# Kernel tuning notes

Hardware: AMD Instinct MI355X
Metric: run time of the kernel (lower is better)

The kernel has to match this reference:

```python
import jax, jax.numpy as jnp
import numpy as np

B, T, C, H = 4, 2048, 1024, 16

def setup_inputs() -> dict:
    key = jax.random.key(0)
    k1, k2, k3, k4, k5 = jax.random.split(key, 5)
    s = 1.0 / np.sqrt(C)
    return {
        "x": jax.random.normal(k1, (B, T, C), dtype=jnp.float32),
        "w_attn": jax.random.normal(k2, (C, 3 * C), dtype=jnp.float32) * s,
        "b_attn": jax.random.normal(k3, (3 * C,), dtype=jnp.float32) * 0.02,
        "w_proj": jax.random.normal(k4, (C, C), dtype=jnp.float32) * s,
        "b_proj": jax.random.normal(k5, (C,), dtype=jnp.float32) * 0.02,
    }

def reference(x, w_attn, b_attn, w_proj, b_proj):
    Bx, Tx, Cx = x.shape
    hd = Cx // H  # head_size
    qkv = x @ w_attn + b_attn                      # [B,T,3C]
    q, k, v = jnp.split(qkv, 3, axis=2)
    # [B,T,C] -> [B,H,T,hd]
    def heads(t):
        return t.reshape(Bx, Tx, H, hd).transpose(0, 2, 1, 3)
    q, k, v = heads(q), heads(k), heads(v)
    scale = hd ** -0.5
    scores = jnp.einsum("bhqd,bhkd->bhqk", q, k) * scale  # [B,H,T,T]
    causal = jnp.tril(jnp.ones((Tx, Tx), dtype=bool))
    scores = jnp.where(causal[None, None], scores, -jnp.inf)
    probs = jax.nn.softmax(scores, axis=-1)
    attn = jnp.einsum("bhqk,bhkd->bhqd", probs, v)  # [B,H,T,hd]
    attn = attn.transpose(0, 2, 1, 3).reshape(Bx, Tx, Cx)
    return attn @ w_proj + b_proj
```

## Files before the change

### kernel.cpp

```cpp
#include <hip/hip_runtime.h>
#include <hip/hip_bf16.h>

#define BATCH 4
#define TSEQ  2048
#define CDIM  1024
#define NHEAD 16
#define HDIM  64
#define C3    3072
#define MROWS (BATCH * TSEQ)

#define QSCALE 0.18033688011112f

typedef short bf16x8 __attribute__((ext_vector_type(8)));
typedef short short8 __attribute__((ext_vector_type(8)));
typedef __bf16 bf16v8 __attribute__((ext_vector_type(8)));
typedef float f32x4 __attribute__((ext_vector_type(4)));

#define AS1 __attribute__((address_space(1)))
#define AS3 __attribute__((address_space(3)))

#if __has_builtin(__builtin_amdgcn_exp2f)
#define EXP2F(x) __builtin_amdgcn_exp2f(x)
#else
#define EXP2F(x) exp2f(x)
#endif

__device__ __forceinline__ short f2bf(float x) {
    unsigned int u = __builtin_bit_cast(unsigned int, x);
    u += 0x7fffu + ((u >> 16) & 1u);
    return (short)(u >> 16);
}

__device__ __forceinline__ unsigned int cvtpk(float lo, float hi) {
    unsigned int r;
    asm("v_cvt_pk_bf16_f32 %0, %1, %2" : "=v"(r) : "v"(lo), "v"(hi));
    return r;
}

__device__ __forceinline__ f32x4 mfma16(bf16x8 a, bf16x8 b, f32x4 c) {
    return __builtin_amdgcn_mfma_f32_16x16x32_bf16(
        __builtin_bit_cast(bf16v8, a), __builtin_bit_cast(bf16v8, b), c, 0, 0, 0);
}

__global__ void f32_to_bf16_kernel(const float* __restrict__ in,
                                   short* __restrict__ out, int n8) {
    int i = blockIdx.x * blockDim.x + threadIdx.x;
    if (i >= n8) return;
    float4 a = ((const float4*)in)[2 * i];
    float4 b = ((const float4*)in)[2 * i + 1];
    short8 o;
    o[0] = f2bf(a.x); o[1] = f2bf(a.y); o[2] = f2bf(a.z); o[3] = f2bf(a.w);
    o[4] = f2bf(b.x); o[5] = f2bf(b.y); o[6] = f2bf(b.z); o[7] = f2bf(b.w);
    ((short8*)out)[i] = o;
}

__global__ void transpose2_kernel(const float* __restrict__ wA,
                                  short* __restrict__ wAT,
                                  const float* __restrict__ wP,
                                  short* __restrict__ wPT, float qs) {
    const float* in;
    short* out;
    int N, qcols;
    float sc;
    if (blockIdx.z == 0) { in = wA; out = wAT; N = C3; qcols = CDIM; sc = qs; }
    else {
        if (blockIdx.x >= CDIM / 32) return;
        in = wP; out = wPT; N = CDIM; qcols = 0; sc = 1.0f;
    }
    __shared__ float tile[32][33];
    const int n0 = blockIdx.x * 32, k0 = blockIdx.y * 32;
    const int tx = threadIdx.x, ty = threadIdx.y;
#pragma unroll
    for (int j = 0; j < 4; ++j)
        tile[ty + j * 8][tx] = in[(size_t)(k0 + ty + j * 8) * N + n0 + tx];
    __syncthreads();
#pragma unroll
    for (int j = 0; j < 4; ++j) {
        const int n = n0 + ty + j * 8;
        const float s = (n < qcols) ? sc : 1.0f;
        out[(size_t)n * CDIM + k0 + tx] = f2bf(tile[tx][ty + j * 8] * s);
    }
}

template <typename OutT, int WAVES_M, int WAVES_N, int BN>
__global__ __launch_bounds__(512, 4) void gemm3_kernel(
    const short* __restrict__ A, const short* __restrict__ Bt,
    const float* __restrict__ bias, OutT* __restrict__ out,
    int M, int N, int K, int qcols, float qs) {
    constexpr int BM = 128;
    constexpr int MF = BM / (WAVES_M * 16);
    constexpr int NF = BN / (WAVES_N * 16);
    constexpr int BLOADS = BN / 128;
    __shared__ alignas(16) short Ab[3][BM * 32];
    __shared__ alignas(16) short Bb[3][BN * 32];

    const int tid = threadIdx.x;
    const int lane = tid & 63;
    const int w = tid >> 6;
    const int wm = w / WAVES_N;
    const int wn = w % WAVES_N;

    const int nwg = gridDim.x * gridDim.y;
    const int lid = blockIdx.y * gridDim.x + blockIdx.x;
    const int swz = (lid & 7) * (nwg >> 3) + (lid >> 3);
    const int m0 = (swz / gridDim.x) * BM;
    const int n0 = (swz % gridDim.x) * BN;

    const int NT = K >> 5;

    const int fr = lane & 15;
    const int ch = lane >> 4;

    f32x4 acc[MF][NF] = {};

    const int rA  = tid >> 2;
    const int lcA = (tid & 3) ^ ((rA >> 1) & 3);
    const short* gA = A + (size_t)(m0 + rA) * K + lcA * 8;
    const short* gB[BLOADS];
#pragma unroll
    for (int i = 0; i < BLOADS; ++i) {
        const int s = tid + i * 512;
        const int r = s >> 2;
        const int lc = (s & 3) ^ ((r >> 1) & 3);
        gB[i] = Bt + (size_t)(n0 + r) * K + lc * 8;
    }

    int aoff[MF], boff[NF];
#pragma unroll
    for (int f = 0; f < MF; ++f) {
        const int r = wm * (BM / WAVES_M) + f * 16 + fr;
        aoff[f] = r * 32 + (ch ^ ((r >> 1) & 3)) * 8;
    }
#pragma unroll
    for (int f = 0; f < NF; ++f) {
        const int r = wn * (BN / WAVES_N) + f * 16 + fr;
        boff[f] = r * 32 + (ch ^ ((r >> 1) & 3)) * 8;
    }

#define GSTAGE(buf, kt)                                                          \
    do {                                                                         \
        __builtin_amdgcn_global_load_lds((const AS1 void*)(gA + (kt)),           \
            (AS3 void*)&Ab[buf][w * 512], 16, 0, 0);                             \
        _Pragma("unroll")                                                        \
        for (int i = 0; i < BLOADS; ++i)                                         \
            __builtin_amdgcn_global_load_lds((const AS1 void*)(gB[i] + (kt)),    \
                (AS3 void*)&Bb[buf][i * 4096 + w * 512], 16, 0, 0);              \
    } while (0)

#define GITER(BUF, T)                                                            \
    do {                                                                         \
        if constexpr (BLOADS == 2) {                                             \
            asm volatile("s_waitcnt vmcnt(3)" ::: "memory");                     \
        } else {                                                                 \
            asm volatile("s_waitcnt vmcnt(2)" ::: "memory");                     \
        }                                                                        \
        __builtin_amdgcn_s_barrier();                                            \
        const int ktn = (((T) + 2 < NT) ? ((T) + 2) : 0) * 32;                   \
        GSTAGE((BUF + 2) % 3, ktn);                                              \
        __builtin_amdgcn_sched_barrier(0);                                       \
        bf16x8 af[MF], bfv[NF];                                                  \
        _Pragma("unroll")                                                        \
        for (int f = 0; f < MF; ++f)                                             \
            af[f] = *(const bf16x8*)&Ab[BUF][aoff[f]];                           \
        _Pragma("unroll")                                                        \
        for (int f = 0; f < NF; ++f)                                             \
            bfv[f] = *(const bf16x8*)&Bb[BUF][boff[f]];                          \
        _Pragma("unroll")                                                        \
        for (int mf = 0; mf < MF; ++mf)                                          \
            _Pragma("unroll")                                                    \
            for (int nf = 0; nf < NF; ++nf)                                      \
                acc[mf][nf] = mfma16(af[mf], bfv[nf], acc[mf][nf]);              \
    } while (0)

    GSTAGE(0, 0);
    GSTAGE(1, 32);

    int t = 0;
    for (; t + 3 <= NT; t += 3) {
        GITER(0, t);
        GITER(1, t + 1);
        GITER(2, t + 2);
    }
    if (t < NT) { GITER(0, t); ++t; }
    if (t < NT) { GITER(1, t); }
#undef GITER
#undef GSTAGE

    const int r0 = (lane >> 4) * 4;
    const int cn = lane & 15;
#pragma unroll
    for (int mf = 0; mf < MF; ++mf) {
#pragma unroll
        for (int nf = 0; nf < NF; ++nf) {
            const int col = n0 + wn * (BN / WAVES_N) + nf * 16 + cn;
            const float bv = bias[col] * ((col < qcols) ? qs : 1.0f);
#pragma unroll
            for (int r = 0; r < 4; ++r) {
                const int row = m0 + wm * (BM / WAVES_M) + mf * 16 + r0 + r;
                const float v = acc[mf][nf][r] + bv;
                if constexpr (sizeof(OutT) == 2)
                    out[(size_t)row * N + col] = (OutT)f2bf(v);
                else
                    out[(size_t)row * N + col] = (OutT)v;
            }
        }
    }
}

template <int BUF>
__device__ __forceinline__ void attn_iter(
    int KB, int niter, int qrow, int w, int cn, int g, int kg8,
    int krow, int kx0, int kx1, int skv, int sd0,
    const short* kgl, size_t ksrc, const short* vbase,
    short (*klds)[64 * 64], short (*vt)[64 * 72],
    const bf16x8 (&qf)[2][2], f32x4 (&ao)[2][4], f32x4 (&ao4)[2],
    const bf16x8& vones) {

    const int kvb = KB * 64;
    const bool pf = (KB + 1 < niter);

    bf16x8 r0, r1;
    if (pf) {
        r0 = *(const bf16x8*)(vbase + (size_t)(kvb + 64 + skv) * C3 + sd0);
        r1 = *(const bf16x8*)(vbase + (size_t)(kvb + 64 + skv + 1) * C3 + sd0);
        const short* kn = kgl + ksrc + (size_t)(kvb + 64) * C3;
        __builtin_amdgcn_global_load_lds((const AS1 void*)kn,
            (AS3 void*)&klds[BUF ^ 1][w * 512], 16, 0, 0);
        __builtin_amdgcn_global_load_lds((const AS1 void*)(kn + (size_t)32 * C3),
            (AS3 void*)&klds[BUF ^ 1][2048 + w * 512], 16, 0, 0);
    }

    if (kvb <= qrow + 31) {
        bf16x8 kf[4][2];
#pragma unroll
        for (int t = 0; t < 4; ++t) {
            const int rb = t * 1024 + krow;
            kf[t][0] = *(const bf16x8*)&klds[BUF][rb + kx0];
            kf[t][1] = *(const bf16x8*)&klds[BUF][rb + kx1];
        }

        bf16x8 vf[2][4];
#pragma unroll
        for (int c = 0; c < 2; ++c)
#pragma unroll
            for (int dt = 0; dt < 4; ++dt)
                vf[c][dt] = *(const bf16x8*)&vt[BUF][(dt * 16 + cn) * 72 + c * 32 + kg8];

#pragma unroll
        for (int qt = 0; qt < 2; ++qt) {
            const int qrow16 = qrow + qt * 16;

            f32x4 s[4] = {};
#pragma unroll
            for (int t = 0; t < 4; ++t) {
                s[t] = mfma16(kf[t][0], qf[qt][0], s[t]);
                s[t] = mfma16(kf[t][1], qf[qt][1], s[t]);
            }

            const bool maskIter = (kvb + 63 > qrow16);
            float p[4][4];
            if (maskIter) {
#pragma unroll
                for (int t = 0; t < 4; ++t)
#pragma unroll
                    for (int r = 0; r < 4; ++r) {
                        const int kv = kvb + t * 16 + 4 * g + r;
                        const int q  = qrow16 + cn;
                        float e = EXP2F(s[t][r]);
                        p[t][r] = (kv > q) ? 0.f : e;
                    }
            } else {
#pragma unroll
                for (int t = 0; t < 4; ++t)
#pragma unroll
                    for (int r = 0; r < 4; ++r)
                        p[t][r] = EXP2F(s[t][r]);
            }

            unsigned int wq[8];
#pragma unroll
            for (int t = 0; t < 4; ++t) {
                wq[t * 2 + 0] = cvtpk(p[t][0], p[t][1]);
                wq[t * 2 + 1] = cvtpk(p[t][2], p[t][3]);
            }

#pragma unroll
            for (int c = 0; c < 2; ++c) {
                union { unsigned int u[4]; bf16x8 v; } pu;
                unsigned int p0 = wq[4 * c + 0], p2 = wq[4 * c + 2];
                asm("v_permlane32_swap_b32 %0, %1" : "+v"(p0), "+v"(p2));
                asm("v_permlane16_swap_b32 %0, %1" : "+v"(p0), "+v"(p2));
                pu.u[0] = p0; pu.u[2] = p2;
                unsigned int p1 = wq[4 * c + 1], p3 = wq[4 * c + 3];
                asm("v_permlane32_swap_b32 %0, %1" : "+v"(p1), "+v"(p3));
                asm("v_permlane16_swap_b32 %0, %1" : "+v"(p1), "+v"(p3));
                pu.u[1] = p1; pu.u[3] = p3;
#pragma unroll
                for (int dt = 0; dt < 4; ++dt)
                    ao[qt][dt] = mfma16(pu.v, vf[c][dt], ao[qt][dt]);
                ao4[qt] = mfma16(pu.v, vones, ao4[qt]);
            }
        }
    }

    if (pf) {
#pragma unroll
        for (int i = 0; i < 8; ++i) {
            unsigned int pk = (unsigned short)r0[i] | ((unsigned int)(unsigned short)r1[i] << 16);
            *(unsigned int*)&vt[BUF ^ 1][(sd0 + i) * 72 + skv] = pk;
        }
    }
    __syncthreads();
}

__global__ __launch_bounds__(256) void attn_kernel(const short* __restrict__ qkv,
                                                   short* __restrict__ attn_out) {
    __shared__ short vt[2][64 * 72];
    __shared__ short klds[2][64 * 64];

    const int tid = threadIdx.x;
    const int lane = tid & 63;
    const int w = tid >> 6;

    const int bid = blockIdx.x;
    const int swz = (bid & 7) * 64 + (bid >> 3);
    const int bh = swz >> 3;
    const int pairp = swz & 7;
    const int b = bh >> 4;
    const int h = bh & 15;

    const size_t base = (size_t)b * TSEQ * C3 + (size_t)h * HDIM;
    const int cn = lane & 15;
    const int g = lane >> 4;
    const int kg8 = g * 8;

    const bf16x8 vones = {0x3F80, 0x3F80, 0x3F80, 0x3F80,
                          0x3F80, 0x3F80, 0x3F80, 0x3F80};

    const short* kgl = qkv + base + 1024;
    const size_t ksrc = (size_t)(w * 8 + (lane >> 3)) * C3 + ((lane & 7) ^ (lane >> 3)) * 8;
    const int cnl = cn & 7;
    const int krow = cn * 64;
    const int kx0 = ((g ^ cnl) * 8);
    const int kx1 = (((g ^ 4) ^ cnl) * 8);

    const int skv = (tid & 31) * 2;
    const int sd0 = (tid >> 5) * 8;
    const short* vbase = qkv + base + 2048;

    for (int pass = 0; pass < 2; ++pass) {
        const int qi = pass ? pairp : (15 - pairp);
        const int q0 = qi * 128;
        const int qrow = q0 + w * 32;
        const int niter = 2 * qi + 2;

        bf16x8 qf[2][2];
#pragma unroll
        for (int qt = 0; qt < 2; ++qt)
#pragma unroll
            for (int ks = 0; ks < 2; ++ks)
                qf[qt][ks] = *(const bf16x8*)(qkv + base +
                    (size_t)(qrow + qt * 16 + cn) * C3 + ks * 32 + kg8);

        f32x4 ao[2][4] = {};
        f32x4 ao4[2] = {};

        {
            __builtin_amdgcn_global_load_lds((const AS1 void*)(kgl + ksrc),
                                             (AS3 void*)&klds[0][w * 512], 16, 0, 0);
            __builtin_amdgcn_global_load_lds((const AS1 void*)(kgl + ksrc + (size_t)32 * C3),
                                             (AS3 void*)&klds[0][2048 + w * 512], 16, 0, 0);
            bf16x8 r0 = *(const bf16x8*)(vbase + (size_t)skv * C3 + sd0);
            bf16x8 r1 = *(const bf16x8*)(vbase + (size_t)(skv + 1) * C3 + sd0);
#pragma unroll
            for (int i = 0; i < 8; ++i) {
                unsigned int pk = (unsigned short)r0[i] | ((unsigned int)(unsigned short)r1[i] << 16);
                *(unsigned int*)&vt[0][(sd0 + i) * 72 + skv] = pk;
            }
        }
        __syncthreads();

        int kb = 0;
        for (; kb + 2 <= niter; kb += 2) {
            attn_iter<0>(kb,     niter, qrow, w, cn, g, kg8, krow, kx0, kx1,
                         skv, sd0, kgl, ksrc, vbase, klds, vt, qf, ao, ao4, vones);
            attn_iter<1>(kb + 1, niter, qrow, w, cn, g, kg8, krow, kx0, kx1,
                         skv, sd0, kgl, ksrc, vbase, klds, vt, qf, ao, ao4, vones);
        }

#pragma unroll
        for (int qt = 0; qt < 2; ++qt) {
#pragma unroll
            for (int r = 0; r < 4; ++r) {
                const float lr = 1.0f / ao4[qt][r];
                const int q = qrow + qt * 16 + 4 * g + r;
#pragma unroll
                for (int dt = 0; dt < 4; ++dt)
                    attn_out[(size_t)(b * TSEQ + q) * CDIM + h * HDIM + dt * 16 + cn] =
                        f2bf(ao[qt][dt][r] * lr);
            }
        }
        __syncthreads();
    }
}

extern "C" void kernel_launch(void* const* d_in, const int* in_sizes, int n_in,
                              void* d_out, int out_size, void* d_ws, size_t ws_size,
                              hipStream_t stream) {
    const float* x      = (const float*)d_in[0];
    const float* w_attn = (const float*)d_in[1];
    const float* b_attn = (const float*)d_in[2];
    const float* w_proj = (const float*)d_in[3];
    const float* b_proj = (const float*)d_in[4];
    float* out = (float*)d_out;

    char* ws = (char*)d_ws;
    short* x_bf   = (short*)ws;
    short* wqkvT  = (short*)(ws + (16u << 20));
    short* wprojT = (short*)(ws + (22u << 20));
    short* qkv    = (short*)(ws + (24u << 20));

    f32_to_bf16_kernel<<<(MROWS * CDIM / 8 + 255) / 256, 256, 0, stream>>>(x, x_bf, MROWS * CDIM / 8);
    transpose2_kernel<<<dim3(C3 / 32, CDIM / 32, 2), dim3(32, 8), 0, stream>>>(
        w_attn, wqkvT, w_proj, wprojT, QSCALE);

    gemm3_kernel<short, 2, 4, 256><<<dim3(C3 / 256, MROWS / 128), 512, 0, stream>>>(
        x_bf, wqkvT, b_attn, qkv, MROWS, C3, CDIM, CDIM, QSCALE);

    attn_kernel<<<dim3(512), 256, 0, stream>>>(qkv, x_bf);

    gemm3_kernel<float, 4, 2, 128><<<dim3(CDIM / 128, MROWS / 128), 512, 0, stream>>>(
        x_bf, wprojT, b_proj, out, MROWS, CDIM, CDIM, 0, 1.0f);
}
```

Measured before the change: 160.0 us.

## Add 256x128-tile GEMM kernel with workgroup swizzle for QKV projection

Adds a new GEMM kernel with 4 waves per 256-thread block, each computing a 128x64 sub-tile (8x4 MFMA fragments) of a 256x128 block tile. Loading uses triple-buffered direct global-to-LDS copies with XOR swizzling. Block indices are remapped with a modulo-8 swizzle for cache locality. The QKV projection now uses it in place of the 512-thread 128x256 kernel, aiming for more register-level reuse per wave. The cost is much higher register pressure and fewer waves per CU.

```diff
diff --git a/kernel.cpp b/kernel.cpp
--- a/kernel.cpp
+++ b/kernel.cpp
@@ -82,6 +82,130 @@
     }
 }
 
+template <typename OutT>
+__global__ __launch_bounds__(256, 2) void gemm4_kernel(
+    const short* __restrict__ A, const short* __restrict__ Bt,
+    const float* __restrict__ bias, OutT* __restrict__ out,
+    int M, int N, int K, int qcols, float qs) {
+    constexpr int MF = 8, NF = 4;
+    __shared__ alignas(16) short Ab[3][256 * 32];
+    __shared__ alignas(16) short Bb[3][128 * 32];
+
+    const int tid = threadIdx.x;
+    const int lane = tid & 63;
+    const int w = tid >> 6;
+    const int wm = w >> 1, wn = w & 1;
+
+    const int nwg = gridDim.x * gridDim.y;
+    const int lid = blockIdx.y * gridDim.x + blockIdx.x;
+    const int swz = (lid & 7) * (nwg >> 3) + (lid >> 3);
+    const int m0 = (swz / gridDim.x) * 256;
+    const int n0 = (swz % gridDim.x) * 128;
+
+    const int NT = K >> 5;
+
+    const int fr = lane & 15;
+    const int ch = lane >> 4;
+
+    f32x4 acc[MF][NF] = {};
+
+    const short* gA[4];
+#pragma unroll
+    for (int i = 0; i < 4; ++i) {
+        const int s = tid + i * 256;
+        const int r = s >> 2;
+        const int lc = (s & 3) ^ ((r >> 1) & 3);
+        gA[i] = A + (size_t)(m0 + r) * K + lc * 8;
+    }
+    const short* gB[2];
+#pragma unroll
+    for (int i = 0; i < 2; ++i) {
+        const int s = tid + i * 256;
+        const int r = s >> 2;
+        const int lc = (s & 3) ^ ((r >> 1) & 3);
+        gB[i] = Bt + (size_t)(n0 + r) * K + lc * 8;
+    }
+
+    int aoff[MF], boff[NF];
+#pragma unroll
+    for (int f = 0; f < MF; ++f) {
+        const int r = wm * 128 + f * 16 + fr;
+        aoff[f] = r * 32 + (ch ^ ((r >> 1) & 3)) * 8;
+    }
+#pragma unroll
+    for (int f = 0; f < NF; ++f) {
+        const int r = wn * 64 + f * 16 + fr;
+        boff[f] = r * 32 + (ch ^ ((r >> 1) & 3)) * 8;
+    }
+
+#define G4STAGE(buf, kt)                                                         \
+    do {                                                                         \
+        _Pragma("unroll")                                                        \
+        for (int i = 0; i < 4; ++i)                                              \
+            __builtin_amdgcn_global_load_lds((const AS1 void*)(gA[i] + (kt)),    \
+                (AS3 void*)&Ab[buf][i * 2048 + w * 512], 16, 0, 0);              \
+        _Pragma("unroll")                                                        \
+        for (int i = 0; i < 2; ++i)                                              \
+            __builtin_amdgcn_global_load_lds((const AS1 void*)(gB[i] + (kt)),    \
+                (AS3 void*)&Bb[buf][i * 2048 + w * 512], 16, 0, 0);              \
+    } while (0)
+
+#define G4ITER(BUF, T)                                                           \
+    do {                                                                         \
+        asm volatile("s_waitcnt vmcnt(6)" ::: "memory");                         \
+        __builtin_amdgcn_s_barrier();                                            \
+        const int ktn = (((T) + 2 < NT) ? ((T) + 2) : 0) * 32;                   \
+        G4STAGE((BUF + 2) % 3, ktn);                                             \
+        __builtin_amdgcn_sched_barrier(0);                                       \
+        bf16x8 af[MF], bfv[NF];                                                  \
+        _Pragma("unroll")                                                        \
+        for (int f = 0; f < MF; ++f)                                             \
+            af[f] = *(const bf16x8*)&Ab[BUF][aoff[f]];                           \
+        _Pragma("unroll")                                                        \
+        for (int f = 0; f < NF; ++f)                                             \
+            bfv[f] = *(const bf16x8*)&Bb[BUF][boff[f]];                          \
+        _Pragma("unroll")                                                        \
+        for (int mf = 0; mf < MF; ++mf)                                          \
+            _Pragma("unroll")                                                    \
+            for (int nf = 0; nf < NF; ++nf)                                      \
+                acc[mf][nf] = mfma16(af[mf], bfv[nf], acc[mf][nf]);              \
+    } while (0)
+
+    G4STAGE(0, 0);
+    G4STAGE(1, 32);
+
+    int t = 0;
+    for (; t + 3 <= NT; t += 3) {
+        G4ITER(0, t);
+        G4ITER(1, t + 1);
+        G4ITER(2, t + 2);
+    }
+    if (t < NT) { G4ITER(0, t); ++t; }
+    if (t < NT) { G4ITER(1, t); }
+#undef G4ITER
+#undef G4STAGE
+
+    const int r0 = (lane >> 4) * 4;
+    const int cn = lane & 15;
+#pragma unroll
+    for (int mf = 0; mf < MF; ++mf) {
+#pragma unroll
+        for (int nf = 0; nf < NF; ++nf) {
+            const int col = n0 + wn * 64 + nf * 16 + cn;
+            const float bv = bias[col] * ((col < qcols) ? qs : 1.0f);
+#pragma unroll
+            for (int r = 0; r < 4; ++r) {
+                const int row = m0 + wm * 128 + mf * 16 + r0 + r;
+                const float v = acc[mf][nf][r] + bv;
+                if constexpr (sizeof(OutT) == 2)
+                    out[(size_t)row * N + col] = (OutT)f2bf(v);
+                else
+                    out[(size_t)row * N + col] = (OutT)v;
+            }
+        }
+    }
+}
+
 template <typename OutT, int WAVES_M, int WAVES_N, int BN>
 __global__ __launch_bounds__(512, 4) void gemm3_kernel(
     const short* __restrict__ A, const short* __restrict__ Bt,
@@ -424,7 +548,7 @@
     transpose2_kernel<<<dim3(C3 / 32, CDIM / 32, 2), dim3(32, 8), 0, stream>>>(
         w_attn, wqkvT, w_proj, wprojT, QSCALE);
 
-    gemm3_kernel<short, 2, 4, 256><<<dim3(C3 / 256, MROWS / 128), 512, 0, stream>>>(
+    gemm4_kernel<short><<<dim3(C3 / 128, MROWS / 256), 256, 0, stream>>>(
         x_bf, wqkvT, b_attn, qkv, MROWS, C3, CDIM, CDIM, QSCALE);
 
     attn_kernel<<<dim3(512), 256, 0, stream>>>(qkv, x_bf);
```

Result: slower. 163.9 us (+2.5%).

## Restructure attention to 2-wave blocks with 64 query rows per wave; merge prep kernels

Applied to the files above, without the earlier changes.

The attention kernel now launches 1024 blocks of 128 threads, each handling one 128-row query tile with two waves covering 64 rows each, instead of 512 blocks of 4 waves that each processed a paired heavy and light tile in two passes. Each wave now keeps four 16-row query fragments and accumulators, which doubles K/V reuse per LDS load but raises register pressure, and each thread loads twice as much K/V per stage. Blocks are ordered with the heaviest causal tiles first so the scheduler can balance the load. The x-to-bf16 conversion and the weight transposes are merged into one prep launch to save a kernel launch.

```diff
diff --git a/kernel.cpp b/kernel.cpp
--- a/kernel.cpp
+++ b/kernel.cpp
@@ -42,34 +42,34 @@
         __builtin_bit_cast(bf16v8, a), __builtin_bit_cast(bf16v8, b), c, 0, 0, 0);
 }
 
-__global__ void f32_to_bf16_kernel(const float* __restrict__ in,
-                                   short* __restrict__ out, int n8) {
-    int i = blockIdx.x * blockDim.x + threadIdx.x;
-    if (i >= n8) return;
-    float4 a = ((const float4*)in)[2 * i];
-    float4 b = ((const float4*)in)[2 * i + 1];
-    short8 o;
-    o[0] = f2bf(a.x); o[1] = f2bf(a.y); o[2] = f2bf(a.z); o[3] = f2bf(a.w);
-    o[4] = f2bf(b.x); o[5] = f2bf(b.y); o[6] = f2bf(b.z); o[7] = f2bf(b.w);
-    ((short8*)out)[i] = o;
-}
-
-__global__ void transpose2_kernel(const float* __restrict__ wA,
-                                  short* __restrict__ wAT,
-                                  const float* __restrict__ wP,
-                                  short* __restrict__ wPT, float qs) {
+__global__ void prep_kernel(const float* __restrict__ x, short* __restrict__ x_bf,
+                            const float* __restrict__ wA, short* __restrict__ wAT,
+                            const float* __restrict__ wP, short* __restrict__ wPT,
+                            float qs) {
+    const int tx = threadIdx.x, ty = threadIdx.y;
+    if (blockIdx.z == 0) {
+        const int i = (blockIdx.y * 128 + blockIdx.x) * 256 + ty * 32 + tx;
+        float4 a = ((const float4*)x)[2 * i];
+        float4 b = ((const float4*)x)[2 * i + 1];
+        short8 o;
+        o[0] = f2bf(a.x); o[1] = f2bf(a.y); o[2] = f2bf(a.z); o[3] = f2bf(a.w);
+        o[4] = f2bf(b.x); o[5] = f2bf(b.y); o[6] = f2bf(b.z); o[7] = f2bf(b.w);
+        ((short8*)x_bf)[i] = o;
+        return;
+    }
     const float* in;
     short* out;
     int N, qcols;
     float sc;
-    if (blockIdx.z == 0) { in = wA; out = wAT; N = C3; qcols = CDIM; sc = qs; }
-    else {
+    if (blockIdx.z == 1) {
+        if (blockIdx.x >= C3 / 32) return;
+        in = wA; out = wAT; N = C3; qcols = CDIM; sc = qs;
+    } else {
         if (blockIdx.x >= CDIM / 32) return;
         in = wP; out = wPT; N = CDIM; qcols = 0; sc = 1.0f;
     }
     __shared__ float tile[32][33];
     const int n0 = blockIdx.x * 32, k0 = blockIdx.y * 32;
-    const int tx = threadIdx.x, ty = threadIdx.y;
 #pragma unroll
     for (int j = 0; j < 4; ++j)
         tile[ty + j * 8][tx] = in[(size_t)(k0 + ty + j * 8) * N + n0 + tx];
@@ -213,24 +213,28 @@
     int krow, int kx0, int kx1, int skv, int sd0,
     const short* kgl, size_t ksrc, const short* vbase,
     short (*klds)[64 * 64], short (*vt)[64 * 72],
-    const bf16x8 (&qf)[2][2], f32x4 (&ao)[2][4], f32x4 (&ao4)[2],
+    const bf16x8 (&qf)[4][2], f32x4 (&ao)[4][4], f32x4 (&ao4)[4],
     const bf16x8& vones) {
 
     const int kvb = KB * 64;
     const bool pf = (KB + 1 < niter);
 
-    bf16x8 r0, r1;
+    bf16x8 r0, r1, r2, r3;
     if (pf) {
-        r0 = *(const bf16x8*)(vbase + (size_t)(kvb + 64 + skv) * C3 + sd0);
-        r1 = *(const bf16x8*)(vbase + (size_t)(kvb + 64 + skv + 1) * C3 + sd0);
+        const short* vn = vbase + (size_t)(kvb + 64) * C3;
+        r0 = *(const bf16x8*)(vn + (size_t)skv * C3 + sd0);
+        r1 = *(const bf16x8*)(vn + (size_t)(skv + 1) * C3 + sd0);
+        r2 = *(const bf16x8*)(vn + (size_t)skv * C3 + sd0 + 32);
+        r3 = *(const bf16x8*)(vn + (size_t)(skv + 1) * C3 + sd0 + 32);
         const short* kn = kgl + ksrc + (size_t)(kvb + 64) * C3;
-        __builtin_amdgcn_global_load_lds((const AS1 void*)kn,
-            (AS3 void*)&klds[BUF ^ 1][w * 512], 16, 0, 0);
-        __builtin_amdgcn_global_load_lds((const AS1 void*)(kn + (size_t)32 * C3),
-            (AS3 void*)&klds[BUF ^ 1][2048 + w * 512], 16, 0, 0);
-    }
-
-    if (kvb <= qrow + 31) {
+#pragma unroll
+        for (int c = 0; c < 4; ++c)
+            __builtin_amdgcn_global_load_lds(
+                (const AS1 void*)(kn + (size_t)(c * 16) * C3),
+                (AS3 void*)&klds[BUF ^ 1][c * 1024 + w * 512], 16, 0, 0);
+    }
+
+    if (kvb <= qrow + 63) {
         bf16x8 kf[4][2];
 #pragma unroll
         for (int t = 0; t < 4; ++t) {
@@ -247,7 +251,7 @@
                 vf[c][dt] = *(const bf16x8*)&vt[BUF][(dt * 16 + cn) * 72 + c * 32 + kg8];
 
 #pragma unroll
-        for (int qt = 0; qt < 2; ++qt) {
+        for (int qt = 0; qt < 4; ++qt) {
             const int qrow16 = qrow + qt * 16;
 
             f32x4 s[4] = {};
@@ -306,14 +310,16 @@
     if (pf) {
 #pragma unroll
         for (int i = 0; i < 8; ++i) {
-            unsigned int pk = (unsigned short)r0[i] | ((unsigned int)(unsigned short)r1[i] << 16);
-            *(unsigned int*)&vt[BUF ^ 1][(sd0 + i) * 72 + skv] = pk;
+            unsigned int pkA = (unsigned short)r0[i] | ((unsigned int)(unsigned short)r1[i] << 16);
+            unsigned int pkB = (unsigned short)r2[i] | ((unsigned int)(unsigned short)r3[i] << 16);
+            *(unsigned int*)&vt[BUF ^ 1][(sd0 + i) * 72 + skv] = pkA;
+            *(unsigned int*)&vt[BUF ^ 1][(sd0 + 32 + i) * 72 + skv] = pkB;
         }
     }
     __syncthreads();
 }
 
-__global__ __launch_bounds__(256) void attn_kernel(const short* __restrict__ qkv,
+__global__ __launch_bounds__(128) void attn_kernel(const short* __restrict__ qkv,
                                                    short* __restrict__ attn_out) {
     __shared__ short vt[2][64 * 72];
     __shared__ short klds[2][64 * 64];
@@ -323,9 +329,8 @@
     const int w = tid >> 6;
 
     const int bid = blockIdx.x;
-    const int swz = (bid & 7) * 64 + (bid >> 3);
-    const int bh = swz >> 3;
-    const int pairp = swz & 7;
+    const int qi = 15 - (bid >> 6);
+    const int bh = (bid & 7) * 8 + ((bid >> 3) & 7);
     const int b = bh >> 4;
     const int h = bh & 15;
 
@@ -348,59 +353,60 @@
     const int sd0 = (tid >> 5) * 8;
     const short* vbase = qkv + base + 2048;
 
-    for (int pass = 0; pass < 2; ++pass) {
-        const int qi = pass ? pairp : (15 - pairp);
-        const int q0 = qi * 128;
-        const int qrow = q0 + w * 32;
-        const int niter = 2 * qi + 2;
-
-        bf16x8 qf[2][2];
-#pragma unroll
-        for (int qt = 0; qt < 2; ++qt)
-#pragma unroll
-            for (int ks = 0; ks < 2; ++ks)
-                qf[qt][ks] = *(const bf16x8*)(qkv + base +
-                    (size_t)(qrow + qt * 16 + cn) * C3 + ks * 32 + kg8);
-
-        f32x4 ao[2][4] = {};
-        f32x4 ao4[2] = {};
-
-        {
-            __builtin_amdgcn_global_load_lds((const AS1 void*)(kgl + ksrc),
-                                             (AS3 void*)&klds[0][w * 512], 16, 0, 0);
-            __builtin_amdgcn_global_load_lds((const AS1 void*)(kgl + ksrc + (size_t)32 * C3),
-                                             (AS3 void*)&klds[0][2048 + w * 512], 16, 0, 0);
-            bf16x8 r0 = *(const bf16x8*)(vbase + (size_t)skv * C3 + sd0);
-            bf16x8 r1 = *(const bf16x8*)(vbase + (size_t)(skv + 1) * C3 + sd0);
-#pragma unroll
-            for (int i = 0; i < 8; ++i) {
-                unsigned int pk = (unsigned short)r0[i] | ((unsigned int)(unsigned short)r1[i] << 16);
-                *(unsigned int*)&vt[0][(sd0 + i) * 72 + skv] = pk;
-            }
-        }
-        __syncthreads();
-
-        int kb = 0;
-        for (; kb + 2 <= niter; kb += 2) {
-            attn_iter<0>(kb,     niter, qrow, w, cn, g, kg8, krow, kx0, kx1,
-                         skv, sd0, kgl, ksrc, vbase, klds, vt, qf, ao, ao4, vones);
-            attn_iter<1>(kb + 1, niter, qrow, w, cn, g, kg8, krow, kx0, kx1,
-                         skv, sd0, kgl, ksrc, vbase, klds, vt, qf, ao, ao4, vones);
-        }
-
-#pragma unroll
-        for (int qt = 0; qt < 2; ++qt) {
-#pragma unroll
-            for (int r = 0; r < 4; ++r) {
-                const float lr = 1.0f / ao4[qt][r];
-                const int q = qrow + qt * 16 + 4 * g + r;
-#pragma unroll
-                for (int dt = 0; dt < 4; ++dt)
-                    attn_out[(size_t)(b * TSEQ + q) * CDIM + h * HDIM + dt * 16 + cn] =
-                        f2bf(ao[qt][dt][r] * lr);
-            }
-        }
-        __syncthreads();
+    const int q0 = qi * 128;
+    const int qrow = q0 + w * 64;
+    const int niter = 2 * qi + 2;
+
+    bf16x8 qf[4][2];
+#pragma unroll
+    for (int qt = 0; qt < 4; ++qt)
+#pragma unroll
+        for (int ks = 0; ks < 2; ++ks)
+            qf[qt][ks] = *(const bf16x8*)(qkv + base +
+                (size_t)(qrow + qt * 16 + cn) * C3 + ks * 32 + kg8);
+
+    f32x4 ao[4][4] = {};
+    f32x4 ao4[4] = {};
+
+    {
+#pragma unroll
+        for (int c = 0; c < 4; ++c)
+            __builtin_amdgcn_global_load_lds(
+                (const AS1 void*)(kgl + ksrc + (size_t)(c * 16) * C3),
+                (AS3 void*)&klds[0][c * 1024 + w * 512], 16, 0, 0);
+        bf16x8 r0 = *(const bf16x8*)(vbase + (size_t)skv * C3 + sd0);
+        bf16x8 r1 = *(const bf16x8*)(vbase + (size_t)(skv + 1) * C3 + sd0);
+        bf16x8 r2 = *(const bf16x8*)(vbase + (size_t)skv * C3 + sd0 + 32);
+        bf16x8 r3 = *(const bf16x8*)(vbase + (size_t)(skv + 1) * C3 + sd0 + 32);
+#pragma unroll
+        for (int i = 0; i < 8; ++i) {
+            unsigned int pkA = (unsigned short)r0[i] | ((unsigned int)(unsigned short)r1[i] << 16);
+            unsigned int pkB = (unsigned short)r2[i] | ((unsigned int)(unsigned short)r3[i] << 16);
+            *(unsigned int*)&vt[0][(sd0 + i) * 72 + skv] = pkA;
+            *(unsigned int*)&vt[0][(sd0 + 32 + i) * 72 + skv] = pkB;
+        }
+    }
+    __syncthreads();
+
+    int kb = 0;
+    for (; kb + 2 <= niter; kb += 2) {
+        attn_iter<0>(kb,     niter, qrow, w, cn, g, kg8, krow, kx0, kx1,
+                     skv, sd0, kgl, ksrc, vbase, klds, vt, qf, ao, ao4, vones);
+        attn_iter<1>(kb + 1, niter, qrow, w, cn, g, kg8, krow, kx0, kx1,
+                     skv, sd0, kgl, ksrc, vbase, klds, vt, qf, ao, ao4, vones);
+    }
+
+#pragma unroll
+    for (int qt = 0; qt < 4; ++qt) {
+#pragma unroll
+        for (int r = 0; r < 4; ++r) {
+            const float lr = 1.0f / ao4[qt][r];
+            const int q = qrow + qt * 16 + 4 * g + r;
+#pragma unroll
+            for (int dt = 0; dt < 4; ++dt)
+                attn_out[(size_t)(b * TSEQ + q) * CDIM + h * HDIM + dt * 16 + cn] =
+                    f2bf(ao[qt][dt][r] * lr);
+        }
     }
 }
 
@@ -420,14 +426,13 @@
     short* wprojT = (short*)(ws + (22u << 20));
     short* qkv    = (short*)(ws + (24u << 20));
 
-    f32_to_bf16_kernel<<<(MROWS * CDIM / 8 + 255) / 256, 256, 0, stream>>>(x, x_bf, MROWS * CDIM / 8);
-    transpose2_kernel<<<dim3(C3 / 32, CDIM / 32, 2), dim3(32, 8), 0, stream>>>(
-        w_attn, wqkvT, w_proj, wprojT, QSCALE);
+    prep_kernel<<<dim3(128, 32, 3), dim3(32, 8), 0, stream>>>(
+        x, x_bf, w_attn, wqkvT, w_proj, wprojT, QSCALE);
 
     gemm3_kernel<short, 2, 4, 256><<<dim3(C3 / 256, MROWS / 128), 512, 0, stream>>>(
         x_bf, wqkvT, b_attn, qkv, MROWS, C3, CDIM, CDIM, QSCALE);
 
-    attn_kernel<<<dim3(512), 256, 0, stream>>>(qkv, x_bf);
+    attn_kernel<<<dim3(1024), 128, 0, stream>>>(qkv, x_bf);
 
     gemm3_kernel<float, 4, 2, 128><<<dim3(CDIM / 128, MROWS / 128), 512, 0, stream>>>(
         x_bf, wprojT, b_proj, out, MROWS, CDIM, CDIM, 0, 1.0f);
```

Result: slower. 163.4 us (+2.1%).
